# Kernel optimization log

Hardware: AMD Instinct MI355X
Metric: run time of the kernel (lower is better)

Reference implementation:

```python
import jax, jax.numpy as jnp
import numpy as np

B, C, H, W = 8, 128, 64, 64
C8, C2 = C // 8, C // 2


def conv1x1(x, w, b):
    # x: [B,Cin,H,W], w: [Cout,Cin], b: [Cout]
    return jnp.einsum('bchw,oc->bohw', x, w) + b[None, :, None, None]


def maxpool2(x):
    # 2x2 stride-2 max pool on [B,C,H,W]
    b, c, h, w = x.shape
    return x.reshape(b, c, h // 2, 2, w // 2, 2).max(axis=(3, 5))


def setup_inputs() -> dict:
    key = jax.random.key(0)
    ks = jax.random.split(key, 10)
    s_in = 1.0 / np.sqrt(C)
    s_c2 = 1.0 / np.sqrt(C2)
    return {
        'x': jax.random.normal(ks[0], (B, C, H, W), dtype=jnp.float32),
        'w_theta': jax.random.uniform(ks[1], (C8, C), jnp.float32, -s_in, s_in),
        'b_theta': jax.random.uniform(ks[2], (C8,), jnp.float32, -s_in, s_in),
        'w_phi': jax.random.uniform(ks[3], (C8, C), jnp.float32, -s_in, s_in),
        'b_phi': jax.random.uniform(ks[4], (C8,), jnp.float32, -s_in, s_in),
        'w_g': jax.random.uniform(ks[5], (C2, C), jnp.float32, -s_in, s_in),
        'b_g': jax.random.uniform(ks[6], (C2,), jnp.float32, -s_in, s_in),
        'w_attn': jax.random.uniform(ks[7], (C, C2), jnp.float32, -s_c2, s_c2),
        'b_attn': jax.random.uniform(ks[8], (C,), jnp.float32, -s_c2, s_c2),
        'sigma': jnp.zeros((1,), dtype=jnp.float32),
    }


def reference(x, w_theta, b_theta, w_phi, b_phi, w_g, b_g, w_attn, b_attn, sigma):
    b, ch, h, w = x.shape
    n, m = h * w, (h * w) // 4
    theta = conv1x1(x, w_theta, b_theta).reshape(b, ch // 8, n)          # [B,C8,N]
    phi = maxpool2(conv1x1(x, w_phi, b_phi)).reshape(b, ch // 8, m)      # [B,C8,M]
    attn = jax.nn.softmax(jnp.einsum('bdn,bdm->bnm', theta, phi), axis=-1)  # [B,N,M]
    g = maxpool2(conv1x1(x, w_g, b_g)).reshape(b, ch // 2, m)            # [B,C2,M]
    attn_g = jnp.einsum('bcm,bnm->bcn', g, attn).reshape(b, ch // 2, h, w)
    attn_g = conv1x1(attn_g, w_attn, b_attn)
    return x + sigma[0] * attn_g
```

## Files before the change

kernel.cpp:

```cpp
#include <hip/hip_runtime.h>
#include <math.h>

#define Bn 8
#define Cn 128
#define Nn 4096
#define Mn 1024
#define C8n 16
#define C2n 64

typedef __attribute__((ext_vector_type(8))) short short8;
typedef __attribute__((ext_vector_type(4))) float floatx4;

__device__ __forceinline__ unsigned short f2bf(float f) {
    union { float f; unsigned u; } v; v.f = f;
    unsigned r = v.u + 0x7fff + ((v.u >> 16) & 1);
    return (unsigned short)(r >> 16);
}

__global__ __launch_bounds__(1024) void k1_pre(
    const float* __restrict__ x,
    const float* __restrict__ w_theta, const float* __restrict__ b_theta,
    const float* __restrict__ w_phi,   const float* __restrict__ b_phi,
    const float* __restrict__ w_g,     const float* __restrict__ b_g,
    unsigned short* __restrict__ thA,
    unsigned short* __restrict__ phB,
    unsigned short* __restrict__ gB)
{
    __shared__ float xs[128][128];
    __shared__ float ws[80][128];
    __shared__ float wt[16][128];
    const int bx = blockIdx.x;
    const int b  = bx & 7;
    const int h2 = bx >> 3;
    const int t  = threadIdx.x;

    const float* xb = x + (size_t)b * Cn * Nn + h2 * 128;
    #pragma unroll
    for (int k = 0; k < 4; ++k) {
        int i = t + k * 1024;
        int c = i >> 5, p4 = i & 31;
        *(float4*)&xs[c][p4 * 4] = *(const float4*)(xb + (size_t)c * Nn + p4 * 4);
    }
    #pragma unroll
    for (int k = 0; k < 3; ++k) {
        int i = t + k * 1024;
        if (i < 2560) {
            int r = i >> 5, c4 = i & 31;
            float4 v = (r < C8n) ? *(const float4*)(w_phi + r * Cn + c4 * 4)
                                 : *(const float4*)(w_g + (r - C8n) * Cn + c4 * 4);
            *(float4*)&ws[r][c4 * 4] = v;
        }
    }
    if (t < 512) {
        int r = t >> 5, c4 = t & 31;
        *(float4*)&wt[r][c4 * 4] = *(const float4*)(w_theta + r * Cn + c4 * 4);
    }
    __syncthreads();

    if (t < 640) {
        const int oc0 = (t >> 5) * 4;
        const int w2  = t & 31;
        const int p   = 2 * w2;
        float a[4][4];
        #pragma unroll
        for (int q = 0; q < 4; ++q) { a[q][0]=0.f; a[q][1]=0.f; a[q][2]=0.f; a[q][3]=0.f; }
        for (int c = 0; c < 128; c += 4) {
            float2 e[4][2];
            #pragma unroll
            for (int cq = 0; cq < 4; ++cq) {
                e[cq][0] = *(float2*)&xs[c + cq][p];
                e[cq][1] = *(float2*)&xs[c + cq][p + 64];
            }
            #pragma unroll
            for (int q = 0; q < 4; ++q) {
                float4 wv = *(float4*)&ws[oc0 + q][c];
                a[q][0] = fmaf(wv.x, e[0][0].x, a[q][0]); a[q][1] = fmaf(wv.x, e[0][0].y, a[q][1]);
                a[q][2] = fmaf(wv.x, e[0][1].x, a[q][2]); a[q][3] = fmaf(wv.x, e[0][1].y, a[q][3]);
                a[q][0] = fmaf(wv.y, e[1][0].x, a[q][0]); a[q][1] = fmaf(wv.y, e[1][0].y, a[q][1]);
                a[q][2] = fmaf(wv.y, e[1][1].x, a[q][2]); a[q][3] = fmaf(wv.y, e[1][1].y, a[q][3]);
                a[q][0] = fmaf(wv.z, e[2][0].x, a[q][0]); a[q][1] = fmaf(wv.z, e[2][0].y, a[q][1]);
                a[q][2] = fmaf(wv.z, e[2][1].x, a[q][2]); a[q][3] = fmaf(wv.z, e[2][1].y, a[q][3]);
                a[q][0] = fmaf(wv.w, e[3][0].x, a[q][0]); a[q][1] = fmaf(wv.w, e[3][0].y, a[q][1]);
                a[q][2] = fmaf(wv.w, e[3][1].x, a[q][2]); a[q][3] = fmaf(wv.w, e[3][1].y, a[q][3]);
            }
        }
        #pragma unroll
        for (int q = 0; q < 4; ++q) {
            const int oc = oc0 + q;
            float bias = (oc < C8n) ? b_phi[oc] : b_g[oc - C8n];
            float r = fmaxf(fmaxf(a[q][0], a[q][1]), fmaxf(a[q][2], a[q][3])) + bias;
            unsigned short hv = f2bf(r);
            if (oc < C8n) {
                int mt = h2 * 2 + (w2 >> 4), ml = w2 & 15;
                phB[(((size_t)b * 64 + mt) * 2 + (oc >> 3)) * 128 + ml * 8 + (oc & 7)] = hv;
            } else {
                int c = oc - C8n;
                int s = ((w2 & 15) << 1) | (w2 >> 4);
                gB[((((size_t)b * 32 + h2) * 4 + (c >> 4)) * 4 + (s >> 3)) * 128
                   + (c & 15) * 8 + (s & 7)] = hv;
            }
        }
    } else {
        #pragma unroll
        for (int k = 0; k < 2; ++k) {
            int u = (t - 640) + k * 384;
            if (u < 512) {
                int d = u >> 5, n4 = u & 31;
                float acc0 = 0.f, acc1 = 0.f, acc2 = 0.f, acc3 = 0.f;
                for (int c = 0; c < 128; ++c) {
                    float wv = wt[d][c];
                    float4 xv = *(float4*)&xs[c][n4 * 4];
                    acc0 = fmaf(wv, xv.x, acc0); acc1 = fmaf(wv, xv.y, acc1);
                    acc2 = fmaf(wv, xv.z, acc2); acc3 = fmaf(wv, xv.w, acc3);
                }
                float bt = b_theta[d];
                const float LOG2E = 1.4426950408889634f;
                float tv[4] = { (acc0 + bt) * LOG2E, (acc1 + bt) * LOG2E,
                                (acc2 + bt) * LOG2E, (acc3 + bt) * LOG2E };
                #pragma unroll
                for (int j = 0; j < 4; ++j) {
                    int ng = h2 * 128 + n4 * 4 + j;
                    thA[(((size_t)b * 256 + (ng >> 4)) * 2 + (d >> 3)) * 128
                        + (ng & 15) * 8 + (d & 7)] = f2bf(tv[j]);
                }
            }
        }
    }
}

__global__ __launch_bounds__(256, 2) void k2_attn(
    const float* __restrict__ x,
    const unsigned short* __restrict__ thA,
    const unsigned short* __restrict__ phB,
    const unsigned short* __restrict__ gB,
    const float* __restrict__ w_attn, const float* __restrict__ b_attn,
    const float* __restrict__ sigma_p,
    float* __restrict__ out)
{
    __shared__ float smem[18816];
    unsigned short* phis = (unsigned short*)smem;
    unsigned short* gs   = (unsigned short*)smem + 4096;
    char* Pall = (char*)smem + 40960;
    float* battn = (float*)((char*)smem + 74752);

    const int tid  = threadIdx.x;
    const int wave = tid >> 6;
    const int lane = tid & 63;
    const int q    = lane >> 4;
    const int l15  = lane & 15;
    const int b    = blockIdx.x & 7;
    const int n0   = (blockIdx.x >> 3) * 64;
    const int nw   = n0 + wave * 16;
    char* Pbase = Pall + wave * 8448;

    const float sg = sigma_p[0];

    short8 thf = {};
    if (q < 2)
        thf = *(const short8*)(thA + ((((size_t)b * 256 + (nw >> 4)) * 2 + q) * 16 + l15) * 8);

    floatx4 O[4];
    #pragma unroll
    for (int cs = 0; cs < 4; ++cs) O[cs] = (floatx4){0.f, 0.f, 0.f, 0.f};
    float L[4]    = {0.f, 0.f, 0.f, 0.f};
    float rmax[4] = {-1e30f, -1e30f, -1e30f, -1e30f};

    for (int s = 0; s < 4; ++s) {
        __syncthreads();
        {
            const float4* psrc = (const float4*)(phB + ((size_t)b * 64 + s * 16) * 256);
            const float4* gsrc = (const float4*)(gB + ((size_t)b * 32 + s * 8) * 2048);
            #pragma unroll
            for (int k = 0; k < 10; ++k) {
                int i = tid + k * 256;
                if (i < 512) ((float4*)smem)[i] = psrc[i];
                else ((float4*)((char*)smem + 8192))[i - 512] = gsrc[i - 512];
            }
        }
        __syncthreads();

        floatx4 S[16];
        #pragma unroll
        for (int mt = 0; mt < 16; ++mt) {
            short8 bf = {};
            if (q < 2) bf = *(const short8*)(phis + ((mt * 2 + q) * 16 + l15) * 8);
            S[mt] = __builtin_amdgcn_mfma_f32_16x16x32_bf16(
                        thf, bf, (floatx4){0.f, 0.f, 0.f, 0.f}, 0, 0, 0);
        }

        float cm[4];
        #pragma unroll
        for (int r = 0; r < 4; ++r) cm[r] = S[0][r];
        #pragma unroll
        for (int mt = 1; mt < 16; ++mt)
            #pragma unroll
            for (int r = 0; r < 4; ++r) cm[r] = fmaxf(cm[r], S[mt][r]);
        #pragma unroll
        for (int d = 1; d <= 8; d <<= 1)
            #pragma unroll
            for (int r = 0; r < 4; ++r) cm[r] = fmaxf(cm[r], __shfl_xor(cm[r], d, 64));
        float f[4];
        #pragma unroll
        for (int r = 0; r < 4; ++r) {
            float nm = fmaxf(rmax[r], cm[r]);
            f[r] = exp2f(rmax[r] - nm);
            rmax[r] = nm;
            L[r] *= f[r];
        }
        #pragma unroll
        for (int cs = 0; cs < 4; ++cs)
            #pragma unroll
            for (int r = 0; r < 4; ++r) O[cs][r] *= f[r];

        #pragma unroll
        for (int g2 = 0; g2 < 8; ++g2) {
            #pragma unroll
            for (int r = 0; r < 4; ++r) {
                float pa = exp2f(S[2 * g2][r]     - rmax[r]);
                float pb = exp2f(S[2 * g2 + 1][r] - rmax[r]);
                L[r] += pa + pb;
                unsigned dw = (unsigned)f2bf(pa) | ((unsigned)f2bf(pb) << 16);
                *(unsigned*)(Pbase + (q * 4 + r) * 528 + g2 * 64 + l15 * 4) = dw;
            }
        }
        __syncthreads();

        #pragma unroll
        for (int ch = 0; ch < 8; ++ch) {
            short8 Af = *(const short8*)(Pbase + l15 * 528 + ch * 64 + q * 16);
            const unsigned short* gchunk = gs + ch * 2048;
            #pragma unroll
            for (int cs = 0; cs < 4; ++cs) {
                short8 Bf = *(const short8*)(gchunk + ((cs * 4 + q) * 16 + l15) * 8);
                O[cs] = __builtin_amdgcn_mfma_f32_16x16x32_bf16(Af, Bf, O[cs], 0, 0, 0);
            }
        }
    }

    __syncthreads();
    {
        unsigned short* wA = (unsigned short*)smem;
        #pragma unroll
        for (int k = 0; k < 8; ++k) {
            int i = tid + k * 256;
            float4 wv = ((const float4*)w_attn)[i];
            int o = i >> 4, c4 = (i & 15) * 4;
            float vv[4] = {wv.x, wv.y, wv.z, wv.w};
            #pragma unroll
            for (int j = 0; j < 4; ++j) {
                int c = c4 + j;
                wA[((o >> 4) * 2 + (c >> 5)) * 512 + (o & 15) * 32 + (c & 31)] = f2bf(vv[j]);
            }
        }
        if (tid < 128) battn[tid] = b_attn[tid];
    }
    {
        float inv[4];
        #pragma unroll
        for (int r = 0; r < 4; ++r) inv[r] = 1.0f / L[r];
        unsigned short* Ob = (unsigned short*)Pbase;
        #pragma unroll
        for (int cs = 0; cs < 4; ++cs)
            #pragma unroll
            for (int r = 0; r < 4; ++r)
                Ob[(q * 4 + r) * 72 + cs * 16 + l15] = f2bf(O[cs][r] * inv[r]);
    }
    __syncthreads();

    {
        unsigned short* wA = (unsigned short*)smem;
        unsigned short* Ob = (unsigned short*)Pbase;
        short8 B0 = *(const short8*)(Ob + l15 * 72 + q * 8);
        short8 B1 = *(const short8*)(Ob + l15 * 72 + 32 + q * 8);
        const float* xw = x   + (size_t)b * Cn * Nn + nw + l15;
        float*       ow = out + (size_t)b * Cn * Nn + nw + l15;
        #pragma unroll
        for (int ot = 0; ot < 8; ++ot) {
            short8 A0 = *(const short8*)(wA + (ot * 2 + 0) * 512 + l15 * 32 + q * 8);
            short8 A1 = *(const short8*)(wA + (ot * 2 + 1) * 512 + l15 * 32 + q * 8);
            floatx4 D = __builtin_amdgcn_mfma_f32_16x16x32_bf16(
                            A0, B0, (floatx4){0.f, 0.f, 0.f, 0.f}, 0, 0, 0);
            D = __builtin_amdgcn_mfma_f32_16x16x32_bf16(A1, B1, D, 0, 0, 0);
            #pragma unroll
            for (int r = 0; r < 4; ++r) {
                int o = ot * 16 + q * 4 + r;
                float v = D[r] + battn[o];
                ow[(size_t)o * Nn] = xw[(size_t)o * Nn] + sg * v;
            }
        }
    }
}

extern "C" void kernel_launch(void* const* d_in, const int* in_sizes, int n_in,
                              void* d_out, int out_size, void* d_ws, size_t ws_size,
                              hipStream_t stream) {
    const float* x       = (const float*)d_in[0];
    const float* w_theta = (const float*)d_in[1];
    const float* b_theta = (const float*)d_in[2];
    const float* w_phi   = (const float*)d_in[3];
    const float* b_phi   = (const float*)d_in[4];
    const float* w_g     = (const float*)d_in[5];
    const float* b_g     = (const float*)d_in[6];
    const float* w_attn  = (const float*)d_in[7];
    const float* b_attn  = (const float*)d_in[8];
    const float* sigma   = (const float*)d_in[9];
    float* out = (float*)d_out;

    unsigned short* thA = (unsigned short*)d_ws;
    unsigned short* phB = thA + 524288;
    unsigned short* gBp = phB + 131072;

    k1_pre<<<256, 1024, 0, stream>>>(x, w_theta, b_theta, w_phi, b_phi,
                                     w_g, b_g, thA, phB, gBp);
    k2_attn<<<512, 256, 0, stream>>>(x, thA, phB, gBp, w_attn, b_attn, sigma, out);
}
```

Measured before the change: 121.0 us.

## Rewrite projection kernel with bf16 MFMA and pooled LDS staging

The first kernel's scalar fp32 FMA 1x1 convolutions for theta/phi/g become bf16 MFMA 16x16x32 tiles. It now runs 256-thread blocks and converts x and the weights to bf16 in LDS in MFMA-friendly layouts. Max pooling uses lane shuffles plus a small LDS pool buffer, and outputs are written as vectorized packed stores. This cuts the FMA-bound cost and LDS traffic of the old projection kernel, at the cost of rounding inputs to bf16 before the convolution, which slightly reduces precision.

New measurement: 117.1 us. 1.03x faster.

```diff
diff --git a/kernel.cpp b/kernel.cpp
--- a/kernel.cpp
+++ b/kernel.cpp
@@ -10,6 +10,7 @@
 
 typedef __attribute__((ext_vector_type(8))) short short8;
 typedef __attribute__((ext_vector_type(4))) float floatx4;
+typedef __attribute__((ext_vector_type(4))) unsigned short ushortx4;
 
 __device__ __forceinline__ unsigned short f2bf(float f) {
     union { float f; unsigned u; } v; v.f = f;
@@ -17,7 +18,7 @@
     return (unsigned short)(r >> 16);
 }
 
-__global__ __launch_bounds__(1024) void k1_pre(
+__global__ __launch_bounds__(256) void k1_pre(
     const float* __restrict__ x,
     const float* __restrict__ w_theta, const float* __restrict__ b_theta,
     const float* __restrict__ w_phi,   const float* __restrict__ b_phi,
@@ -26,105 +27,124 @@
     unsigned short* __restrict__ phB,
     unsigned short* __restrict__ gB)
 {
-    __shared__ float xs[128][128];
-    __shared__ float ws[80][128];
-    __shared__ float wt[16][128];
-    const int bx = blockIdx.x;
-    const int b  = bx & 7;
-    const int h2 = bx >> 3;
-    const int t  = threadIdx.x;
+    __shared__ unsigned short wA[6 * 4 * 64 * 8];
+    __shared__ unsigned short xB[8 * 4 * 64 * 8];
+    __shared__ unsigned short pool[80][33];
+    __shared__ float biases[96];
+
+    const int t    = threadIdx.x;
+    const int b    = blockIdx.x & 7;
+    const int h2   = blockIdx.x >> 3;
+    const int wv   = t >> 6;
+    const int lane = t & 63;
+    const int q    = lane >> 4;
+    const int l15  = lane & 15;
+    const float L2E = 1.4426950408889634f;
+
+    if (t < 96)
+        biases[t] = (t < 16) ? b_theta[t] * L2E
+                  : (t < 32) ? b_phi[t - 16] : b_g[t - 32];
+
+    #pragma unroll
+    for (int k = 0; k < 12; ++k) {
+        int u  = t + k * 256;
+        int oc = u >> 5, c4 = u & 31;
+        const float* src = (oc < 16) ? (w_theta + oc * Cn)
+                         : (oc < 32) ? (w_phi + (oc - 16) * Cn)
+                                     : (w_g + (oc - 32) * Cn);
+        float4 wv4 = *(const float4*)(src + c4 * 4);
+        float sc = (oc < 16) ? L2E : 1.f;
+        int c = c4 * 4;
+        int ot = oc >> 4, kc = c >> 5, qq = (c >> 3) & 3, jj = c & 7;
+        ushortx4 pk = { f2bf(wv4.x * sc), f2bf(wv4.y * sc),
+                        f2bf(wv4.z * sc), f2bf(wv4.w * sc) };
+        *(ushortx4*)(wA + (((ot * 4 + kc) * 64 + qq * 16 + (oc & 15)) * 8 + jj)) = pk;
+    }
 
     const float* xb = x + (size_t)b * Cn * Nn + h2 * 128;
     #pragma unroll
-    for (int k = 0; k < 4; ++k) {
-        int i = t + k * 1024;
-        int c = i >> 5, p4 = i & 31;
-        *(float4*)&xs[c][p4 * 4] = *(const float4*)(xb + (size_t)c * Nn + p4 * 4);
-    }
-    #pragma unroll
-    for (int k = 0; k < 3; ++k) {
-        int i = t + k * 1024;
-        if (i < 2560) {
-            int r = i >> 5, c4 = i & 31;
-            float4 v = (r < C8n) ? *(const float4*)(w_phi + r * Cn + c4 * 4)
-                                 : *(const float4*)(w_g + (r - C8n) * Cn + c4 * 4);
-            *(float4*)&ws[r][c4 * 4] = v;
-        }
-    }
-    if (t < 512) {
-        int r = t >> 5, c4 = t & 31;
-        *(float4*)&wt[r][c4 * 4] = *(const float4*)(w_theta + r * Cn + c4 * 4);
+    for (int k = 0; k < 16; ++k) {
+        int u   = t + k * 256;
+        int pos = u & 127, c4 = u >> 7;
+        int c   = c4 * 4;
+        float v0 = xb[(size_t)(c + 0) * Nn + pos];
+        float v1 = xb[(size_t)(c + 1) * Nn + pos];
+        float v2 = xb[(size_t)(c + 2) * Nn + pos];
+        float v3 = xb[(size_t)(c + 3) * Nn + pos];
+        int pt = pos >> 4, kc = c >> 5, qq = (c >> 3) & 3, jj = c & 7;
+        ushortx4 pk = { f2bf(v0), f2bf(v1), f2bf(v2), f2bf(v3) };
+        *(ushortx4*)(xB + (((pt * 4 + kc) * 64 + qq * 16 + (pos & 15)) * 8 + jj)) = pk;
     }
     __syncthreads();
 
-    if (t < 640) {
-        const int oc0 = (t >> 5) * 4;
-        const int w2  = t & 31;
-        const int p   = 2 * w2;
-        float a[4][4];
-        #pragma unroll
-        for (int q = 0; q < 4; ++q) { a[q][0]=0.f; a[q][1]=0.f; a[q][2]=0.f; a[q][3]=0.f; }
-        for (int c = 0; c < 128; c += 4) {
-            float2 e[4][2];
-            #pragma unroll
-            for (int cq = 0; cq < 4; ++cq) {
-                e[cq][0] = *(float2*)&xs[c + cq][p];
-                e[cq][1] = *(float2*)&xs[c + cq][p + 64];
-            }
-            #pragma unroll
-            for (int q = 0; q < 4; ++q) {
-                float4 wv = *(float4*)&ws[oc0 + q][c];
-                a[q][0] = fmaf(wv.x, e[0][0].x, a[q][0]); a[q][1] = fmaf(wv.x, e[0][0].y, a[q][1]);
-                a[q][2] = fmaf(wv.x, e[0][1].x, a[q][2]); a[q][3] = fmaf(wv.x, e[0][1].y, a[q][3]);
-                a[q][0] = fmaf(wv.y, e[1][0].x, a[q][0]); a[q][1] = fmaf(wv.y, e[1][0].y, a[q][1]);
-                a[q][2] = fmaf(wv.y, e[1][1].x, a[q][2]); a[q][3] = fmaf(wv.y, e[1][1].y, a[q][3]);
-                a[q][0] = fmaf(wv.z, e[2][0].x, a[q][0]); a[q][1] = fmaf(wv.z, e[2][0].y, a[q][1]);
-                a[q][2] = fmaf(wv.z, e[2][1].x, a[q][2]); a[q][3] = fmaf(wv.z, e[2][1].y, a[q][3]);
-                a[q][0] = fmaf(wv.w, e[3][0].x, a[q][0]); a[q][1] = fmaf(wv.w, e[3][0].y, a[q][1]);
-                a[q][2] = fmaf(wv.w, e[3][1].x, a[q][2]); a[q][3] = fmaf(wv.w, e[3][1].y, a[q][3]);
-            }
-        }
-        #pragma unroll
-        for (int q = 0; q < 4; ++q) {
-            const int oc = oc0 + q;
-            float bias = (oc < C8n) ? b_phi[oc] : b_g[oc - C8n];
-            float r = fmaxf(fmaxf(a[q][0], a[q][1]), fmaxf(a[q][2], a[q][3])) + bias;
-            unsigned short hv = f2bf(r);
-            if (oc < C8n) {
-                int mt = h2 * 2 + (w2 >> 4), ml = w2 & 15;
-                phB[(((size_t)b * 64 + mt) * 2 + (oc >> 3)) * 128 + ml * 8 + (oc & 7)] = hv;
-            } else {
-                int c = oc - C8n;
-                int s = ((w2 & 15) << 1) | (w2 >> 4);
-                gB[((((size_t)b * 32 + h2) * 4 + (c >> 4)) * 4 + (s >> 3)) * 128
-                   + (c & 15) * 8 + (s & 7)] = hv;
-            }
-        }
-    } else {
-        #pragma unroll
-        for (int k = 0; k < 2; ++k) {
-            int u = (t - 640) + k * 384;
-            if (u < 512) {
-                int d = u >> 5, n4 = u & 31;
-                float acc0 = 0.f, acc1 = 0.f, acc2 = 0.f, acc3 = 0.f;
-                for (int c = 0; c < 128; ++c) {
-                    float wv = wt[d][c];
-                    float4 xv = *(float4*)&xs[c][n4 * 4];
-                    acc0 = fmaf(wv, xv.x, acc0); acc1 = fmaf(wv, xv.y, acc1);
-                    acc2 = fmaf(wv, xv.z, acc2); acc3 = fmaf(wv, xv.w, acc3);
-                }
-                float bt = b_theta[d];
-                const float LOG2E = 1.4426950408889634f;
-                float tv[4] = { (acc0 + bt) * LOG2E, (acc1 + bt) * LOG2E,
-                                (acc2 + bt) * LOG2E, (acc3 + bt) * LOG2E };
-                #pragma unroll
-                for (int j = 0; j < 4; ++j) {
-                    int ng = h2 * 128 + n4 * 4 + j;
-                    thA[(((size_t)b * 256 + (ng >> 4)) * 2 + (d >> 3)) * 128
-                        + (ng & 15) * 8 + (d & 7)] = f2bf(tv[j]);
-                }
-            }
-        }
+    floatx4 acc[6][2];
+    #pragma unroll
+    for (int ot = 0; ot < 6; ++ot)
+        #pragma unroll
+        for (int p2 = 0; p2 < 2; ++p2) acc[ot][p2] = (floatx4){0.f, 0.f, 0.f, 0.f};
+
+    #pragma unroll
+    for (int kc = 0; kc < 4; ++kc) {
+        short8 Bf0 = *(const short8*)(xB + ((wv * 4 + kc) * 64 + lane) * 8);
+        short8 Bf1 = *(const short8*)(xB + (((wv + 4) * 4 + kc) * 64 + lane) * 8);
+        #pragma unroll
+        for (int ot = 0; ot < 6; ++ot) {
+            short8 Af = *(const short8*)(wA + ((ot * 4 + kc) * 64 + lane) * 8);
+            acc[ot][0] = __builtin_amdgcn_mfma_f32_16x16x32_bf16(Af, Bf0, acc[ot][0], 0, 0, 0);
+            acc[ot][1] = __builtin_amdgcn_mfma_f32_16x16x32_bf16(Af, Bf1, acc[ot][1], 0, 0, 0);
+        }
+    }
+
+    #pragma unroll
+    for (int p2 = 0; p2 < 2; ++p2) {
+        const int pt = wv + p2 * 4;
+        ushortx4 pk;
+        #pragma unroll
+        for (int r = 0; r < 4; ++r)
+            pk[r] = f2bf(acc[0][p2][r] + biases[q * 4 + r]);
+        *(ushortx4*)(thA + ((((size_t)b * 256 + h2 * 8 + pt) * 2 + (q >> 1)) * 128
+                            + l15 * 8 + (q & 1) * 4)) = pk;
+    }
+
+    #pragma unroll
+    for (int ot = 1; ot < 6; ++ot) {
+        #pragma unroll
+        for (int r = 0; r < 4; ++r) {
+            float vmax = fmaxf(acc[ot][0][r], acc[ot][1][r]);
+            float pmax = fmaxf(vmax, __shfl_xor(vmax, 1, 64));
+            if ((l15 & 1) == 0) {
+                int oc = (ot - 1) * 16 + q * 4 + r;
+                int w2 = wv * 8 + (l15 >> 1);
+                pool[oc][w2] = f2bf(pmax + biases[16 + oc]);
+            }
+        }
+    }
+    __syncthreads();
+
+    if (t < 64) {
+        int w2h = t >> 5, ml = (t >> 1) & 15, dh = t & 1;
+        int w2 = w2h * 16 + ml;
+        ushortx4 lo, hi;
+        #pragma unroll
+        for (int j = 0; j < 4; ++j) { lo[j] = pool[dh * 8 + j][w2];
+                                      hi[j] = pool[dh * 8 + 4 + j][w2]; }
+        unsigned short* dst = phB + (((size_t)b * 64 + h2 * 2 + w2h) * 2 + dh) * 128 + ml * 8;
+        *(ushortx4*)dst = lo;
+        *(ushortx4*)(dst + 4) = hi;
+    }
+    {
+        int c = t >> 2, sq = t & 3;
+        ushortx4 lo, hi;
+        #pragma unroll
+        for (int j = 0; j < 8; ++j) {
+            int w2 = (j & 1) * 16 + sq * 4 + (j >> 1);
+            unsigned short v = pool[16 + c][w2];
+            if (j < 4) lo[j] = v; else hi[j - 4] = v;
+        }
+        unsigned short* dst = gB + ((((size_t)b * 32 + h2) * 4 + (c >> 4)) * 4 + sq) * 128
+                              + (c & 15) * 8;
+        *(ushortx4*)dst = lo;
+        *(ushortx4*)(dst + 4) = hi;
     }
 }
 
@@ -239,7 +259,7 @@
 
     __syncthreads();
     {
-        unsigned short* wA = (unsigned short*)smem;
+        unsigned short* wAe = (unsigned short*)smem;
         #pragma unroll
         for (int k = 0; k < 8; ++k) {
             int i = tid + k * 256;
@@ -249,7 +269,7 @@
             #pragma unroll
             for (int j = 0; j < 4; ++j) {
                 int c = c4 + j;
-                wA[((o >> 4) * 2 + (c >> 5)) * 512 + (o & 15) * 32 + (c & 31)] = f2bf(vv[j]);
+                wAe[((o >> 4) * 2 + (c >> 5)) * 512 + (o & 15) * 32 + (c & 31)] = f2bf(vv[j]);
             }
         }
         if (tid < 128) battn[tid] = b_attn[tid];
@@ -268,7 +288,7 @@
     __syncthreads();
 
     {
-        unsigned short* wA = (unsigned short*)smem;
+        unsigned short* wAe = (unsigned short*)smem;
         unsigned short* Ob = (unsigned short*)Pbase;
         short8 B0 = *(const short8*)(Ob + l15 * 72 + q * 8);
         short8 B1 = *(const short8*)(Ob + l15 * 72 + 32 + q * 8);
@@ -276,8 +296,8 @@
         float*       ow = out + (size_t)b * Cn * Nn + nw + l15;
         #pragma unroll
         for (int ot = 0; ot < 8; ++ot) {
-            short8 A0 = *(const short8*)(wA + (ot * 2 + 0) * 512 + l15 * 32 + q * 8);
-            short8 A1 = *(const short8*)(wA + (ot * 2 + 1) * 512 + l15 * 32 + q * 8);
+            short8 A0 = *(const short8*)(wAe + (ot * 2 + 0) * 512 + l15 * 32 + q * 8);
+            short8 A1 = *(const short8*)(wAe + (ot * 2 + 1) * 512 + l15 * 32 + q * 8);
             floatx4 D = __builtin_amdgcn_mfma_f32_16x16x32_bf16(
                             A0, B0, (floatx4){0.f, 0.f, 0.f, 0.f}, 0, 0, 0);
             D = __builtin_amdgcn_mfma_f32_16x16x32_bf16(A1, B1, D, 0, 0, 0);
@@ -310,7 +330,7 @@
     unsigned short* phB = thA + 524288;
     unsigned short* gBp = phB + 131072;
 
-    k1_pre<<<256, 1024, 0, stream>>>(x, w_theta, b_theta, w_phi, b_phi,
-                                     w_g, b_g, thA, phB, gBp);
+    k1_pre<<<256, 256, 0, stream>>>(x, w_theta, b_theta, w_phi, b_phi,
+                                    w_g, b_g, thA, phB, gBp);
     k2_attn<<<512, 256, 0, stream>>>(x, thA, phB, gBp, w_attn, b_attn, sigma, out);
 }
```
